# Optimization experiments

Measured on AMD Instinct MI355X. Metric: run time of the kernel, lower is better.

The kernel has to match this reference:

```python
import jax, jax.numpy as jnp
import numpy as np

ALPHA = 0.01  # LeakyReLU negative slope
NEG_INF = -1e12

def setup_inputs() -> dict:
    key = jax.random.key(0)
    k1, k2, k3, k4 = jax.random.split(key, 4)
    B, N, F_in, F_out = 8, 2048, 256, 128
    inp = jax.random.normal(k1, (B, N, F_in), dtype=jnp.float32)
    adj = jax.random.randint(k2, (B, N, N), 0, 2, dtype=jnp.int32)
    # xavier_uniform with gain=1.414
    limW = 1.414 * np.sqrt(6.0 / (F_in + F_out))
    W = jax.random.uniform(k3, (F_in, F_out), minval=-limW, maxval=limW, dtype=jnp.float32)
    lima = 1.414 * np.sqrt(6.0 / (2 * F_out + 1))
    a = jax.random.uniform(k4, (2 * F_out, 1), minval=-lima, maxval=lima, dtype=jnp.float32)
    return {"inp": inp, "adj": adj, "W": W, "a": a}

def reference(inp, adj, W, a):
    # h: [B, N, F_out]
    h = jnp.matmul(inp, W)
    F_out = W.shape[1]
    # Algebraic split of the attention vector: a = [a1; a2], so
    # e[b,i,j] = leakyrelu(h_i . a1 + h_j . a2)  -- avoids the O(N^2*2F) a_input.
    a1 = a[:F_out, 0]   # [F_out]
    a2 = a[F_out:, 0]   # [F_out]
    s1 = jnp.einsum('bnf,f->bn', h, a1)  # [B, N] source term
    s2 = jnp.einsum('bnf,f->bn', h, a2)  # [B, N] target term
    e = s1[:, :, None] + s2[:, None, :]  # [B, N, N]
    e = jnp.where(e > 0, e, ALPHA * e)   # leaky relu
    scores = jnp.where(adj > 0, e, NEG_INF)
    attention = jax.nn.softmax(scores, axis=2)  # [B, N, N]
    h_prime = jnp.matmul(attention, h)          # [B, N, F_out]
    return jax.nn.relu(h_prime)  # concat=True branch
```

## Files before the change

kernel.cpp:

```cpp
#include <hip/hip_runtime.h>
#include <hip/hip_bf16.h>

#define N_    2048
#define FIN   256
#define FOUT  128
#define ALPHA 0.01f

typedef short bf16x8 __attribute__((ext_vector_type(8)));
typedef float f32x4  __attribute__((ext_vector_type(4)));

static __device__ __forceinline__ unsigned short f2bf(float x) {
    __hip_bfloat16 h = __float2bfloat16(x);
    return *reinterpret_cast<unsigned short*>(&h);
}
static __device__ __forceinline__ float bf2f(unsigned short u) {
    return __uint_as_float(((unsigned)u) << 16);
}

__global__ __launch_bounds__(256) void k_wsplit(
    const float* __restrict__ W, unsigned short* __restrict__ WFhi,
    unsigned short* __restrict__ WFlo)
{
    int idx = blockIdx.x * 256 + threadIdx.x;
    int k = idx >> 7, n = idx & 127;
    float w = W[k * 128 + n];
    unsigned short hi = f2bf(w);
    unsigned short lo = f2bf(w - bf2f(hi));
    int nb = n >> 4, ln = n & 15, ks = k >> 5, lg = (k >> 3) & 3, e = k & 7;
    int off = (((nb * 8 + ks) * 4 + lg) * 16 + ln) * 8 + e;
    WFhi[off] = hi;
    WFlo[off] = lo;
}

__global__ __launch_bounds__(256) void k_pack(
    const int* __restrict__ adj, unsigned int* __restrict__ mask)
{
    __shared__ unsigned char mb[256];
    int row = blockIdx.x;
    int t = threadIdx.x;
    const int4* a4 = reinterpret_cast<const int4*>(adj + (size_t)row * N_) + 2 * t;
    int4 x = a4[0], y = a4[1];
    unsigned byte =
        (unsigned)(x.x > 0) | ((unsigned)(x.y > 0) << 1) |
        ((unsigned)(x.z > 0) << 2) | ((unsigned)(x.w > 0) << 3) |
        ((unsigned)(y.x > 0) << 4) | ((unsigned)(y.y > 0) << 5) |
        ((unsigned)(y.z > 0) << 6) | ((unsigned)(y.w > 0) << 7);
    int S = t >> 2, lg = t & 3;
    mb[lg * 64 + S] = (unsigned char)byte;
    __syncthreads();
    if (t < 16)
        reinterpret_cast<uint4*>(mask)[row * 16 + t] =
            reinterpret_cast<const uint4*>(mb)[t];
}

__global__ __launch_bounds__(256) void k_lin(
    const float* __restrict__ inp,
    const unsigned short* __restrict__ WFhi, const unsigned short* __restrict__ WFlo,
    const float* __restrict__ av, unsigned short* __restrict__ hF,
    float* __restrict__ s1, float* __restrict__ s2)
{
    __shared__ unsigned short Ahi[64 * 256];
    __shared__ unsigned short Alo[64 * 256];

    int g = blockIdx.x;
    int b = g & 7;
    int i0 = (g >> 3) << 6;
    int t = threadIdx.x;

    {
        int row = t >> 2;
        const float* src = inp + ((size_t)(b * N_ + i0 + row)) * FIN + (t & 3) * 64;
#pragma unroll
        for (int gseg = 0; gseg < 8; ++gseg) {
            float4 f0 = *reinterpret_cast<const float4*>(src + gseg * 8);
            float4 f1 = *reinterpret_cast<const float4*>(src + gseg * 8 + 4);
            float f[8] = {f0.x, f0.y, f0.z, f0.w, f1.x, f1.y, f1.z, f1.w};
            bf16x8 hi8, lo8;
#pragma unroll
            for (int e = 0; e < 8; ++e) {
                unsigned short h = f2bf(f[e]);
                hi8[e] = (short)h;
                lo8[e] = (short)f2bf(f[e] - bf2f(h));
            }
            int k = (t & 3) * 64 + gseg * 8;
            int off = (row * 512 + k * 2) ^ ((row & 7) << 4);
            *reinterpret_cast<bf16x8*>(reinterpret_cast<char*>(Ahi) + off) = hi8;
            *reinterpret_cast<bf16x8*>(reinterpret_cast<char*>(Alo) + off) = lo8;
        }
    }
    __syncthreads();

    int w = t >> 6, l = t & 63;
    int ln = l & 15, lg = l >> 4;
    const bf16x8* Wh8 = reinterpret_cast<const bf16x8*>(WFhi);
    const bf16x8* Wl8 = reinterpret_cast<const bf16x8*>(WFlo);

    f32x4 acc[8];
#pragma unroll
    for (int nb = 0; nb < 8; ++nb) acc[nb] = (f32x4){0.f, 0.f, 0.f, 0.f};

#pragma unroll
    for (int ks = 0; ks < 8; ++ks) {
        int arow = w * 16 + ln;
        int aoff = (arow * 512 + ks * 64 + lg * 16) ^ ((arow & 7) << 4);
        bf16x8 ahi = *reinterpret_cast<const bf16x8*>(reinterpret_cast<const char*>(Ahi) + aoff);
        bf16x8 alo = *reinterpret_cast<const bf16x8*>(reinterpret_cast<const char*>(Alo) + aoff);
#pragma unroll
        for (int nb = 0; nb < 8; ++nb) {
            int fi = ((nb * 8 + ks) * 4 + lg) * 16 + ln;
            bf16x8 whi = Wh8[fi];
            bf16x8 wlo = Wl8[fi];
            acc[nb] = __builtin_amdgcn_mfma_f32_16x16x32_bf16(ahi, whi, acc[nb], 0, 0, 0);
            acc[nb] = __builtin_amdgcn_mfma_f32_16x16x32_bf16(alo, whi, acc[nb], 0, 0, 0);
            acc[nb] = __builtin_amdgcn_mfma_f32_16x16x32_bf16(ahi, wlo, acc[nb], 0, 0, 0);
        }
    }

    float p1[4] = {0.f, 0.f, 0.f, 0.f}, p2[4] = {0.f, 0.f, 0.f, 0.f};
#pragma unroll
    for (int nb = 0; nb < 8; ++nb) {
        float a1 = av[nb * 16 + ln];
        float a2 = av[FOUT + nb * 16 + ln];
#pragma unroll
        for (int j = 0; j < 4; ++j) {
            p1[j] = fmaf(acc[nb][j], a1, p1[j]);
            p2[j] = fmaf(acc[nb][j], a2, p2[j]);
        }
    }
#pragma unroll
    for (int off = 1; off < 16; off <<= 1)
#pragma unroll
        for (int j = 0; j < 4; ++j) {
            p1[j] += __shfl_xor(p1[j], off);
            p2[j] += __shfl_xor(p2[j], off);
        }
    if (ln == 0) {
#pragma unroll
        for (int j = 0; j < 4; ++j) {
            int row = i0 + w * 16 + lg * 4 + j;
            s1[b * N_ + row] = p1[j];
            s2[b * N_ + row] = p2[j];
        }
    }

    __syncthreads();
    unsigned short* T = Ahi;
#pragma unroll
    for (int nb = 0; nb < 8; ++nb)
#pragma unroll
        for (int j = 0; j < 4; ++j)
            T[(nb * 16 + ln) * 68 + w * 16 + lg * 4 + j] = f2bf(acc[nb][j]);
    __syncthreads();
    {
        int f = t & 127, half = t >> 7;
        int J = (i0 >> 5) + half;
        unsigned short tmp[32];
#pragma unroll
        for (int c = 0; c < 32; ++c) tmp[c] = T[f * 68 + half * 32 + c];
        int4* dst = reinterpret_cast<int4*>(&hF[(((size_t)(b * 64 + J)) * 128 + f) * 32]);
#pragma unroll
        for (int c = 0; c < 4; ++c) dst[c] = reinterpret_cast<const int4*>(tmp)[c];
    }
}

__global__ __launch_bounds__(256) void k_attn(
    const unsigned int* __restrict__ mask, const unsigned short* __restrict__ hF,
    const float* __restrict__ s1g, const float* __restrict__ s2g,
    float* __restrict__ out)
{
    __shared__ float s2_lds[N_];
    __shared__ char  hbuf[2 * 8192];
    __shared__ float red[4];

    int g = blockIdx.x;
    int b = g & 7;
    int i0 = (g >> 3) << 6;
    int t = threadIdx.x;
    int w = t >> 6, l = t & 63;
    int ln = l & 15, lg = l >> 4;

    {
        const float4* s2g4 = reinterpret_cast<const float4*>(s2g + b * N_);
        reinterpret_cast<float4*>(s2_lds)[t] = s2g4[t];
        reinterpret_cast<float4*>(s2_lds)[t + 256] = s2g4[t + 256];
    }

    const int myrow = i0 + w * 16 + ln;
    const float s1r = s1g[b * N_ + myrow];

    const uint4* maskp4 = reinterpret_cast<const uint4*>(
        reinterpret_cast<const char*>(mask) + ((size_t)(b * N_ + myrow)) * 256 + lg * 64);

    const int toff = t * 32;
    const int wbase = toff ^ (((((toff >> 6) ^ (toff >> 8)) & 3)) << 4);
    const int base_r = (ln * 64 + lg * 16) ^ (((ln ^ (ln >> 2)) & 3) << 4);

    const char* hF_b = reinterpret_cast<const char*>(hF) + (size_t)b * 64 * 128 * 64;
    const char* gend = hF_b + 63 * 8192;

    uint4 st[4][2];
#pragma unroll
    for (int k = 0; k < 4; ++k) {
        st[k][0] = *reinterpret_cast<const uint4*>(hF_b + k * 8192 + toff);
        st[k][1] = *reinterpret_cast<const uint4*>(hF_b + k * 8192 + toff + 16);
    }
    *reinterpret_cast<uint4*>(hbuf + wbase) = st[0][0];
    *reinterpret_cast<uint4*>(hbuf + (wbase ^ 16)) = st[0][1];
    st[0][0] = *reinterpret_cast<const uint4*>(hF_b + 4 * 8192 + toff);
    st[0][1] = *reinterpret_cast<const uint4*>(hF_b + 4 * 8192 + toff + 16);
    uint4 mv_cur = maskp4[0];

    asm volatile("s_waitcnt lgkmcnt(0)" ::: "memory");
    __builtin_amdgcn_s_barrier();

    {
        float4 a = *reinterpret_cast<const float4*>(&s2_lds[t * 8]);
        float4 c = *reinterpret_cast<const float4*>(&s2_lds[t * 8 + 4]);
        float m = fmaxf(fmaxf(fmaxf(a.x, a.y), fmaxf(a.z, a.w)),
                        fmaxf(fmaxf(c.x, c.y), fmaxf(c.z, c.w)));
#pragma unroll
        for (int off = 1; off < 64; off <<= 1) m = fmaxf(m, __shfl_xor(m, off));
        if (l == 0) red[w] = m;
        asm volatile("s_waitcnt lgkmcnt(0)" ::: "memory");
        __builtin_amdgcn_s_barrier();
    }
    const float s2m = fmaxf(fmaxf(red[0], red[1]), fmaxf(red[2], red[3]));
    float eb = s1r + s2m;
    const float m_row = fmaxf(eb, ALPHA * eb);

    float l_run = 0.f;
    f32x4 acc[8];
#pragma unroll
    for (int q = 0; q < 8; ++q) acc[q] = (f32x4){0.f, 0.f, 0.f, 0.f};

    const char* gpref = hF_b + 5 * 8192;

    for (int u = 0; u < 4; ++u) {
        uint4 mv_next = maskp4[u < 3 ? u + 1 : 3];
        const float* s2u = &s2_lds[u * 512 + lg * 8];
#pragma unroll
        for (int s = 0; s < 16; ++s) {
            const int cur = s & 1, nxt = cur ^ 1, k = (s + 1) & 3;
            bf16x8 fr[8];
#pragma unroll
            for (int q = 0; q < 8; ++q)
                fr[q] = *reinterpret_cast<const bf16x8*>(hbuf + cur * 8192 + q * 1024 + base_r);
            *reinterpret_cast<uint4*>(hbuf + nxt * 8192 + wbase) = st[k][0];
            *reinterpret_cast<uint4*>(hbuf + nxt * 8192 + (wbase ^ 16)) = st[k][1];
            const char* gp = gpref > gend ? gend : gpref;
            st[k][0] = *reinterpret_cast<const uint4*>(gp + toff);
            st[k][1] = *reinterpret_cast<const uint4*>(gp + toff + 16);
            gpref += 8192;
            unsigned mm = (&mv_cur.x)[s >> 2];
            unsigned byte = (mm >> ((s & 3) * 8)) & 0xffu;
            float4 ca = *reinterpret_cast<const float4*>(s2u + s * 32);
            float4 cb = *reinterpret_cast<const float4*>(s2u + s * 32 + 4);
            float sv[8] = {ca.x, ca.y, ca.z, ca.w, cb.x, cb.y, cb.z, cb.w};
            bf16x8 af;
            float ps = 0.f;
#pragma unroll
            for (int e = 0; e < 8; ++e) {
                float v = s1r + sv[e];
                v = fmaxf(v, ALPHA * v);
                float p = (byte & (1u << e)) ? __expf(v - m_row) : 0.f;
                ps += p;
                af[e] = (short)f2bf(p);
            }
            l_run += ps;
#pragma unroll
            for (int q = 0; q < 8; ++q)
                acc[q] = __builtin_amdgcn_mfma_f32_16x16x32_bf16(af, fr[q], acc[q], 0, 0, 0);
            asm volatile("s_waitcnt lgkmcnt(0)" ::: "memory");
            __builtin_amdgcn_s_barrier();
        }
        mv_cur = mv_next;
    }

    l_run += __shfl_xor(l_run, 16);
    l_run += __shfl_xor(l_run, 32);
    float Lr[4];
#pragma unroll
    for (int rr = 0; rr < 4; ++rr)
        Lr[rr] = __shfl(l_run, lg * 4 + rr);

    float* ob = out + ((size_t)(b * N_ + i0 + w * 16)) * FOUT;
#pragma unroll
    for (int q = 0; q < 8; ++q)
#pragma unroll
        for (int rr = 0; rr < 4; ++rr) {
            float v = acc[q][rr] / Lr[rr];
            ob[(size_t)(lg * 4 + rr) * FOUT + q * 16 + ln] = fmaxf(v, 0.f);
        }
}

extern "C" void kernel_launch(void* const* d_in, const int* in_sizes, int n_in,
                              void* d_out, int out_size, void* d_ws, size_t ws_size,
                              hipStream_t stream) {
    (void)in_sizes; (void)n_in; (void)out_size; (void)ws_size;
    const float* inp = (const float*)d_in[0];
    const int*   adj = (const int*)d_in[1];
    const float* W   = (const float*)d_in[2];
    const float* a   = (const float*)d_in[3];
    float* out = (float*)d_out;

    char* ws = (char*)d_ws;
    unsigned short* hF   = (unsigned short*)ws;
    unsigned int*   mask = (unsigned int*)(ws + (4u << 20));
    float* s1    = (float*)(ws + (8u << 20));
    float* s2    = s1 + 8 * N_;
    unsigned short* WFhi = (unsigned short*)(s2 + 8 * N_);
    unsigned short* WFlo = WFhi + FIN * FOUT;

    k_wsplit<<<128, 256, 0, stream>>>(W, WFhi, WFlo);
    k_pack<<<8 * N_, 256, 0, stream>>>(adj, mask);
    k_lin<<<256, 256, 0, stream>>>(inp, WFhi, WFlo, a, hF, s1, s2);
    k_attn<<<256, 256, 0, stream>>>(mask, hF, s1, s2, out);
}
```

Measured before the change: 278.8 us.

## Load attention h fragments directly from global and batch mask packing rows

k_attn drops the LDS double-buffered staging of h and its per-step barriers, having each lane load its bf16 fragments straight from global memory with register double buffering. It also removes the row-max stabilisation and uses exp(v) directly. k_pack now handles 8 rows per block instead of one. Dropping the max subtraction risks overflow for large logits, and the direct global loads repeat reads across waves that LDS used to share, relying on cache instead.

```diff
diff --git a/kernel.cpp b/kernel.cpp
--- a/kernel.cpp
+++ b/kernel.cpp
@@ -33,23 +33,28 @@
 }
 
 __global__ __launch_bounds__(256) void k_pack(
-    const int* __restrict__ adj, unsigned int* __restrict__ mask)
-{
-    __shared__ unsigned char mb[256];
-    int row = blockIdx.x;
+    const int* __restrict__ adj, unsigned char* __restrict__ mask)
+{
+    __shared__ unsigned char mb[8 * 256];
+    int g = blockIdx.x;
+    size_t row0 = (size_t)g * 8;
     int t = threadIdx.x;
-    const int4* a4 = reinterpret_cast<const int4*>(adj + (size_t)row * N_) + 2 * t;
-    int4 x = a4[0], y = a4[1];
-    unsigned byte =
-        (unsigned)(x.x > 0) | ((unsigned)(x.y > 0) << 1) |
-        ((unsigned)(x.z > 0) << 2) | ((unsigned)(x.w > 0) << 3) |
-        ((unsigned)(y.x > 0) << 4) | ((unsigned)(y.y > 0) << 5) |
-        ((unsigned)(y.z > 0) << 6) | ((unsigned)(y.w > 0) << 7);
     int S = t >> 2, lg = t & 3;
-    mb[lg * 64 + S] = (unsigned char)byte;
-    __syncthreads();
-    if (t < 16)
-        reinterpret_cast<uint4*>(mask)[row * 16 + t] =
+
+#pragma unroll
+    for (int rr = 0; rr < 8; ++rr) {
+        const int4* a4 = reinterpret_cast<const int4*>(adj + (row0 + rr) * N_) + 2 * t;
+        int4 x = a4[0], y = a4[1];
+        unsigned byte =
+            (unsigned)(x.x > 0) | ((unsigned)(x.y > 0) << 1) |
+            ((unsigned)(x.z > 0) << 2) | ((unsigned)(x.w > 0) << 3) |
+            ((unsigned)(y.x > 0) << 4) | ((unsigned)(y.y > 0) << 5) |
+            ((unsigned)(y.z > 0) << 6) | ((unsigned)(y.w > 0) << 7);
+        mb[rr * 256 + lg * 64 + S] = (unsigned char)byte;
+    }
+    __syncthreads();
+    if (t < 128)
+        reinterpret_cast<uint4*>(mask + row0 * 256)[t] =
             reinterpret_cast<const uint4*>(mb)[t];
 }
 
@@ -163,21 +168,19 @@
     }
 }
 
-__global__ __launch_bounds__(256) void k_attn(
-    const unsigned int* __restrict__ mask, const unsigned short* __restrict__ hF,
+__global__ __launch_bounds__(256, 2) void k_attn(
+    const unsigned char* __restrict__ mask, const unsigned short* __restrict__ hF,
     const float* __restrict__ s1g, const float* __restrict__ s2g,
     float* __restrict__ out)
 {
     __shared__ float s2_lds[N_];
-    __shared__ char  hbuf[2 * 8192];
-    __shared__ float red[4];
 
     int g = blockIdx.x;
     int b = g & 7;
     int i0 = (g >> 3) << 6;
     int t = threadIdx.x;
     int w = t >> 6, l = t & 63;
-    int ln = l & 15, lg = l >> 4;
+    int r = l & 15, lg = l >> 4;
 
     {
         const float4* s2g4 = reinterpret_cast<const float4*>(s2g + b * N_);
@@ -185,93 +188,57 @@
         reinterpret_cast<float4*>(s2_lds)[t + 256] = s2g4[t + 256];
     }
 
-    const int myrow = i0 + w * 16 + ln;
+    const int myrow = i0 + w * 16 + r;
     const float s1r = s1g[b * N_ + myrow];
 
-    const uint4* maskp4 = reinterpret_cast<const uint4*>(
-        reinterpret_cast<const char*>(mask) + ((size_t)(b * N_ + myrow)) * 256 + lg * 64);
-
-    const int toff = t * 32;
-    const int wbase = toff ^ (((((toff >> 6) ^ (toff >> 8)) & 3)) << 4);
-    const int base_r = (ln * 64 + lg * 16) ^ (((ln ^ (ln >> 2)) & 3) << 4);
-
-    const char* hF_b = reinterpret_cast<const char*>(hF) + (size_t)b * 64 * 128 * 64;
-    const char* gend = hF_b + 63 * 8192;
-
-    uint4 st[4][2];
-#pragma unroll
-    for (int k = 0; k < 4; ++k) {
-        st[k][0] = *reinterpret_cast<const uint4*>(hF_b + k * 8192 + toff);
-        st[k][1] = *reinterpret_cast<const uint4*>(hF_b + k * 8192 + toff + 16);
-    }
-    *reinterpret_cast<uint4*>(hbuf + wbase) = st[0][0];
-    *reinterpret_cast<uint4*>(hbuf + (wbase ^ 16)) = st[0][1];
-    st[0][0] = *reinterpret_cast<const uint4*>(hF_b + 4 * 8192 + toff);
-    st[0][1] = *reinterpret_cast<const uint4*>(hF_b + 4 * 8192 + toff + 16);
-    uint4 mv_cur = maskp4[0];
-
-    asm volatile("s_waitcnt lgkmcnt(0)" ::: "memory");
-    __builtin_amdgcn_s_barrier();
-
-    {
-        float4 a = *reinterpret_cast<const float4*>(&s2_lds[t * 8]);
-        float4 c = *reinterpret_cast<const float4*>(&s2_lds[t * 8 + 4]);
-        float m = fmaxf(fmaxf(fmaxf(a.x, a.y), fmaxf(a.z, a.w)),
-                        fmaxf(fmaxf(c.x, c.y), fmaxf(c.z, c.w)));
-#pragma unroll
-        for (int off = 1; off < 64; off <<= 1) m = fmaxf(m, __shfl_xor(m, off));
-        if (l == 0) red[w] = m;
-        asm volatile("s_waitcnt lgkmcnt(0)" ::: "memory");
-        __builtin_amdgcn_s_barrier();
-    }
-    const float s2m = fmaxf(fmaxf(red[0], red[1]), fmaxf(red[2], red[3]));
-    float eb = s1r + s2m;
-    const float m_row = fmaxf(eb, ALPHA * eb);
+    const unsigned char* mrow = mask + ((size_t)(b * N_ + myrow)) * 256 + lg * 64;
+
+    const bf16x8* hv = reinterpret_cast<const bf16x8*>(hF)
+        + (((size_t)(b * 64) * 128 + r) * 4 + lg);
 
     float l_run = 0.f;
     f32x4 acc[8];
 #pragma unroll
     for (int q = 0; q < 8; ++q) acc[q] = (f32x4){0.f, 0.f, 0.f, 0.f};
 
-    const char* gpref = hF_b + 5 * 8192;
+    bf16x8 hA[8], hB[8];
+#pragma unroll
+    for (int q = 0; q < 8; ++q) hA[q] = hv[q * 64];
+    uint4 mv_cur = *reinterpret_cast<const uint4*>(mrow);
+
+    __syncthreads();
 
     for (int u = 0; u < 4; ++u) {
-        uint4 mv_next = maskp4[u < 3 ? u + 1 : 3];
-        const float* s2u = &s2_lds[u * 512 + lg * 8];
+        uint4 mv_next = *reinterpret_cast<const uint4*>(mrow + (u < 3 ? (u + 1) * 16 : 48));
 #pragma unroll
         for (int s = 0; s < 16; ++s) {
-            const int cur = s & 1, nxt = cur ^ 1, k = (s + 1) & 3;
-            bf16x8 fr[8];
-#pragma unroll
-            for (int q = 0; q < 8; ++q)
-                fr[q] = *reinterpret_cast<const bf16x8*>(hbuf + cur * 8192 + q * 1024 + base_r);
-            *reinterpret_cast<uint4*>(hbuf + nxt * 8192 + wbase) = st[k][0];
-            *reinterpret_cast<uint4*>(hbuf + nxt * 8192 + (wbase ^ 16)) = st[k][1];
-            const char* gp = gpref > gend ? gend : gpref;
-            st[k][0] = *reinterpret_cast<const uint4*>(gp + toff);
-            st[k][1] = *reinterpret_cast<const uint4*>(gp + toff + 16);
-            gpref += 8192;
-            unsigned mm = (&mv_cur.x)[s >> 2];
-            unsigned byte = (mm >> ((s & 3) * 8)) & 0xffu;
-            float4 ca = *reinterpret_cast<const float4*>(s2u + s * 32);
-            float4 cb = *reinterpret_cast<const float4*>(s2u + s * 32 + 4);
+            const int S = u * 16 + s;
+            auto& cur = (S & 1) ? hB : hA;
+            auto& nxt = (S & 1) ? hA : hB;
+            const int Sn = (S < 63) ? S + 1 : 63;
+#pragma unroll
+            for (int q = 0; q < 8; ++q) nxt[q] = hv[(size_t)Sn * 512 + q * 64];
+
+            unsigned byte = ((&mv_cur.x)[s >> 2] >> ((s & 3) * 8)) & 0xffu;
+            const float* s2b = &s2_lds[S * 32 + lg * 8];
+            float4 ca = *reinterpret_cast<const float4*>(s2b);
+            float4 cb = *reinterpret_cast<const float4*>(s2b + 4);
             float sv[8] = {ca.x, ca.y, ca.z, ca.w, cb.x, cb.y, cb.z, cb.w};
+
             bf16x8 af;
             float ps = 0.f;
 #pragma unroll
             for (int e = 0; e < 8; ++e) {
                 float v = s1r + sv[e];
                 v = fmaxf(v, ALPHA * v);
-                float p = (byte & (1u << e)) ? __expf(v - m_row) : 0.f;
+                float p = (byte & (1u << e)) ? __expf(v) : 0.f;
                 ps += p;
                 af[e] = (short)f2bf(p);
             }
             l_run += ps;
 #pragma unroll
             for (int q = 0; q < 8; ++q)
-                acc[q] = __builtin_amdgcn_mfma_f32_16x16x32_bf16(af, fr[q], acc[q], 0, 0, 0);
-            asm volatile("s_waitcnt lgkmcnt(0)" ::: "memory");
-            __builtin_amdgcn_s_barrier();
+                acc[q] = __builtin_amdgcn_mfma_f32_16x16x32_bf16(af, cur[q], acc[q], 0, 0, 0);
         }
         mv_cur = mv_next;
     }
@@ -289,7 +256,7 @@
 #pragma unroll
         for (int rr = 0; rr < 4; ++rr) {
             float v = acc[q][rr] / Lr[rr];
-            ob[(size_t)(lg * 4 + rr) * FOUT + q * 16 + ln] = fmaxf(v, 0.f);
+            ob[(size_t)(lg * 4 + rr) * FOUT + q * 16 + r] = fmaxf(v, 0.f);
         }
 }
 
@@ -305,14 +272,14 @@
 
     char* ws = (char*)d_ws;
     unsigned short* hF   = (unsigned short*)ws;
-    unsigned int*   mask = (unsigned int*)(ws + (4u << 20));
+    unsigned char*  mask = (unsigned char*)(ws + (4u << 20));
     float* s1    = (float*)(ws + (8u << 20));
     float* s2    = s1 + 8 * N_;
     unsigned short* WFhi = (unsigned short*)(s2 + 8 * N_);
     unsigned short* WFlo = WFhi + FIN * FOUT;
 
     k_wsplit<<<128, 256, 0, stream>>>(W, WFhi, WFlo);
-    k_pack<<<8 * N_, 256, 0, stream>>>(adj, mask);
+    k_pack<<<2048, 256, 0, stream>>>(adj, mask);
     k_lin<<<256, 256, 0, stream>>>(inp, WFhi, WFlo, a, hF, s1, s2);
     k_attn<<<256, 256, 0, stream>>>(mask, hF, s1, s2, out);
 }
```

Result: slower. 323.5 us (+16.0%).
